# Kernel optimization log

Hardware: AMD Instinct MI355X
Metric: run time of the kernel (lower is better)

## Reference

```python
import jax, jax.numpy as jnp
import numpy as np

LATDIM = 128
HEAD = 4
N_NODES = 100000
N_EDGES = 800000

def setup_inputs() -> dict:
    key = jax.random.key(0)
    k1, k2, k3, k4, k5, k6 = jax.random.split(key, 6)
    scale = float(np.sqrt(6.0 / (LATDIM + LATDIM)))  # xavier_uniform bound
    return {
        "rows": jax.random.randint(k1, (N_EDGES,), 0, N_NODES),
        "colEmbeds": jax.random.normal(k2, (N_EDGES, LATDIM), dtype=jnp.float32),
        "embeds": jax.random.normal(k3, (N_NODES, LATDIM), dtype=jnp.float32),
        "qTrans": jax.random.uniform(k4, (LATDIM, LATDIM), minval=-scale, maxval=scale, dtype=jnp.float32),
        "kTrans": jax.random.uniform(k5, (LATDIM, LATDIM), minval=-scale, maxval=scale, dtype=jnp.float32),
        "vTrans": jax.random.uniform(k6, (LATDIM, LATDIM), minval=-scale, maxval=scale, dtype=jnp.float32),
        "shape": N_NODES,
    }

def reference(rows, colEmbeds, embeds, qTrans, kTrans, vTrans, shape):
    d_head = LATDIM // HEAD
    rowEmbeds = embeds[rows]                                   # [E, D] gather
    q = (rowEmbeds @ qTrans).reshape(-1, HEAD, d_head)          # [E, H, d]
    k = (colEmbeds @ kTrans).reshape(-1, HEAD, d_head)          # [E, H, d]
    v = (colEmbeds @ vTrans).reshape(-1, HEAD, d_head)          # [E, H, d]
    att = jnp.einsum('ehd,ehd->eh', q, k)                       # [E, H]
    att = jnp.clip(att, -10.0, 10.0)
    expAtt = jnp.exp(att)
    # segment softmax denominator, broadcast back to edges
    attNorm = jax.ops.segment_sum(expAtt, rows, num_segments=shape)[rows]
    att = expAtt / (attNorm + 1e-8)
    res = (att[:, :, None] * v).reshape(-1, LATDIM)             # [E, D]
    out = jax.ops.segment_sum(res, rows, num_segments=shape)    # [N, D]
    return out
```

## Files before the change

### kernel.cpp

```cpp
#include <hip/hip_runtime.h>
#include <hip/hip_bf16.h>

#define NEDGE 800000
#define NNODE 100000
#define LATD  128
#define NHEAD 4
#define WPAD  136
#define TILES (NEDGE / 16)
#define QTILES (NNODE / 16)
#define NB ((NNODE + 1023) / 1024)

typedef _Float16 half8 __attribute__((ext_vector_type(8)));
typedef _Float16 half4t __attribute__((ext_vector_type(4)));
typedef float    f32x4 __attribute__((ext_vector_type(4)));

__device__ __forceinline__ half8 load_frag_f32(const float* __restrict__ p) {
    const f32x4 a = *reinterpret_cast<const f32x4*>(p);
    const f32x4 b = *reinterpret_cast<const f32x4*>(p + 4);
    half8 r;
    r[0] = (_Float16)a[0]; r[1] = (_Float16)a[1];
    r[2] = (_Float16)a[2]; r[3] = (_Float16)a[3];
    r[4] = (_Float16)b[0]; r[5] = (_Float16)b[1];
    r[6] = (_Float16)b[2]; r[7] = (_Float16)b[3];
    return r;
}

__global__ __launch_bounds__(512, 2) void q_kernel(
    const float* __restrict__ embeds,
    const float* __restrict__ Qw,
    _Float16* __restrict__ qAll)
{
    extern __shared__ _Float16 lds[];
    _Float16* Qt = lds;
    const int t = threadIdx.x;
    for (int idx = t; idx < LATD * LATD; idx += 512) {
        const int d = idx >> 7, c = idx & 127;
        Qt[c * WPAD + d] = (_Float16)Qw[idx];
    }
    __syncthreads();

    const int lane = t & 63;
    const int c16  = lane & 15;
    const int g    = lane >> 4;
    const int wave = (blockIdx.x << 3) + (t >> 6);
    const int nw   = gridDim.x << 3;

    for (int tile = wave; tile < QTILES; tile += nw) {
        const int n0 = tile << 4;
        const float* xrow = embeds + (size_t)(n0 + c16) * LATD + g * 8;
        f32x4 accQ[8] = {};
        #pragma unroll
        for (int ks = 0; ks < 4; ++ks) {
            const half8 ax = load_frag_f32(xrow + ks * 32);
            const int ko = ks * 32 + g * 8;
            #pragma unroll
            for (int nt = 0; nt < 8; ++nt) {
                const half8 bq = *reinterpret_cast<const half8*>(Qt + (nt * 16 + c16) * WPAD + ko);
                accQ[nt] = __builtin_amdgcn_mfma_f32_16x16x32_f16(ax, bq, accQ[nt], 0, 0, 0);
            }
        }
        #pragma unroll
        for (int r = 0; r < 4; ++r) {
            half8 h;
            #pragma unroll
            for (int nt = 0; nt < 8; ++nt) h[nt] = (_Float16)accQ[nt][r];
            *reinterpret_cast<half8*>(qAll + (size_t)(n0 + g * 4 + r) * LATD + c16 * 8) = h;
        }
    }
}

__global__ void hist_kernel(const int* __restrict__ rows, int* __restrict__ counts) {
    const int e = blockIdx.x * 256 + threadIdx.x;
    if (e < NEDGE) atomicAdd(&counts[rows[e]], 1);
}

__global__ __launch_bounds__(1024) void scan1_kernel(
    const int* __restrict__ counts, int* __restrict__ offsets, int* __restrict__ partials)
{
    __shared__ int wt[16];
    __shared__ int wp[16];
    const int b = blockIdx.x;
    const int i = b * 1024 + threadIdx.x;
    const int v = (i < NNODE) ? counts[i] : 0;
    const int lane = threadIdx.x & 63, wid = threadIdx.x >> 6;
    int incl = v;
    #pragma unroll
    for (int d = 1; d < 64; d <<= 1) {
        const int x = __shfl_up(incl, d);
        if (lane >= d) incl += x;
    }
    if (lane == 63) wt[wid] = incl;
    __syncthreads();
    if (threadIdx.x == 0) {
        int s = 0;
        for (int k = 0; k < 16; ++k) { wp[k] = s; s += wt[k]; }
        partials[b] = s;
    }
    __syncthreads();
    if (i < NNODE) offsets[i] = incl - v + wp[wid];
}

__global__ __launch_bounds__(1024) void scan2_kernel(
    int* __restrict__ offsets, int* __restrict__ cursor, const int* __restrict__ partials)
{
    __shared__ int sp[128];
    const int b = blockIdx.x;
    if (threadIdx.x < NB) sp[threadIdx.x] = partials[threadIdx.x];
    __syncthreads();
    int s = 0;
    for (int k = 0; k < b; ++k) s += sp[k];
    const int i = b * 1024 + threadIdx.x;
    if (i < NNODE) {
        const int val = offsets[i] + s;
        offsets[i] = val;
        cursor[i]  = val;
    }
    if (b == 0 && threadIdx.x == 0) offsets[NNODE] = NEDGE;
}

__global__ void scatter_kernel(const int* __restrict__ rows,
                               int* __restrict__ cursor,
                               int* __restrict__ edgeIdx,
                               int* __restrict__ rowsSorted) {
    const int e = blockIdx.x * 256 + threadIdx.x;
    if (e < NEDGE) {
        const int r = rows[e];
        const int p = atomicAdd(&cursor[r], 1);
        edgeIdx[p]    = e;
        rowsSorted[p] = r;
    }
}

__global__ __launch_bounds__(512, 2) void att_kernel(
    const int*      __restrict__ rows,
    const float*    __restrict__ colEmb,
    const _Float16* __restrict__ qAll,
    const float*    __restrict__ Kw,
    _Float16* __restrict__ attN)
{
    extern __shared__ _Float16 lds[];
    _Float16* Kt = lds;
    const int t = threadIdx.x;
    for (int idx = t; idx < LATD * LATD; idx += 512) {
        const int d = idx >> 7, c = idx & 127;
        Kt[c * WPAD + d] = (_Float16)Kw[idx];
    }
    __syncthreads();

    const int lane = t & 63;
    const int c16  = lane & 15;
    const int g    = lane >> 4;
    const int wave = blockIdx.x * 8 + (t >> 6);
    const int nw   = gridDim.x * 8;

    for (int tile = wave; tile < TILES; tile += nw) {
        const int e0 = tile << 4;
        const float* yrow = colEmb + (size_t)(e0 + c16) * LATD + g * 8;

        half8 ay[4];
        #pragma unroll
        for (int ks = 0; ks < 4; ++ks) ay[ks] = load_frag_f32(yrow + ks * 32);

        const int4 rW = *reinterpret_cast<const int4*>(rows + e0 + g * 4);
        half8 qv[4];
        qv[0] = *reinterpret_cast<const half8*>(qAll + (size_t)rW.x * LATD + c16 * 8);
        qv[1] = *reinterpret_cast<const half8*>(qAll + (size_t)rW.y * LATD + c16 * 8);
        qv[2] = *reinterpret_cast<const half8*>(qAll + (size_t)rW.z * LATD + c16 * 8);
        qv[3] = *reinterpret_cast<const half8*>(qAll + (size_t)rW.w * LATD + c16 * 8);

        f32x4 accK[8] = {};
        #pragma unroll
        for (int ks = 0; ks < 4; ++ks) {
            const int ko = ks * 32 + g * 8;
            #pragma unroll
            for (int nt = 0; nt < 8; ++nt) {
                const half8 bk = *reinterpret_cast<const half8*>(Kt + (nt * 16 + c16) * WPAD + ko);
                accK[nt] = __builtin_amdgcn_mfma_f32_16x16x32_f16(ay[ks], bk, accK[nt], 0, 0, 0);
            }
        }

        f32x4 eh[4];
        #pragma unroll
        for (int h = 0; h < 4; ++h) {
            f32x4 p;
            #pragma unroll
            for (int r = 0; r < 4; ++r)
                p[r] = accK[2 * h][r]     * (float)qv[r][2 * h]
                     + accK[2 * h + 1][r] * (float)qv[r][2 * h + 1];
            #pragma unroll
            for (int m = 1; m < 16; m <<= 1) {
                f32x4 q;
                q[0] = __shfl_xor(p[0], m);
                q[1] = __shfl_xor(p[1], m);
                q[2] = __shfl_xor(p[2], m);
                q[3] = __shfl_xor(p[3], m);
                p += q;
            }
            #pragma unroll
            for (int r = 0; r < 4; ++r)
                eh[h][r] = expf(fminf(10.0f, fmaxf(-10.0f, p[r])));
        }

        const f32x4 sel = (c16 == 0) ? eh[0] : (c16 == 1) ? eh[1] : (c16 == 2) ? eh[2] : eh[3];
        if (c16 < NHEAD) {
            #pragma unroll
            for (int r = 0; r < 4; ++r)
                attN[(size_t)(e0 + 4 * g + r) * NHEAD + c16] = (_Float16)sel[r];
        }
    }
}

__global__ __launch_bounds__(512, 2) void pv_kernel(
    const int*      __restrict__ edgeIdx,
    const int*      __restrict__ rowsSorted,
    const float*    __restrict__ colEmb,
    const _Float16* __restrict__ attN,
    const float*    __restrict__ Vw,
    float* __restrict__ outAcc,
    float* __restrict__ attNorm,
    int tilesPerWave)
{
    extern __shared__ _Float16 lds[];
    _Float16* Vt = lds;
    const int t = threadIdx.x;
    for (int idx = t; idx < LATD * LATD; idx += 512) {
        const int d = idx >> 7, c = idx & 127;
        Vt[c * WPAD + d] = (_Float16)Vw[idx];
    }
    __syncthreads();

    const int lane = t & 63;
    const int c16  = lane & 15;
    const int g    = lane >> 4;
    const int wave = blockIdx.x * 8 + (t >> 6);
    const int tile0 = wave * tilesPerWave;
    int tile1 = tile0 + tilesPerWave;
    if (tile1 > TILES) tile1 = TILES;
    if (tile0 >= tile1) return;

    int eA      = edgeIdx[(tile0 << 4) + c16];
    int rid16   = rowsSorted[(tile0 << 4) + c16];
    int4 rB     = *reinterpret_cast<const int4*>(rowsSorted + (tile0 << 4) + g * 4);
    int4 eB     = *reinterpret_cast<const int4*>(edgeIdx    + (tile0 << 4) + g * 4);
    int prevRow = (g == 0) ? -1 : rowsSorted[(tile0 << 4) + 4 * g - 1];

    for (int tile = tile0; tile < tile1; ++tile) {
        const float* yrow = colEmb + (size_t)eA * LATD + g * 8;
        half8 ay[4];
        #pragma unroll
        for (int ks = 0; ks < 4; ++ks) ay[ks] = load_frag_f32(yrow + ks * 32);

        half4t a4[4];
        a4[0] = *reinterpret_cast<const half4t*>(attN + (size_t)eB.x * NHEAD);
        a4[1] = *reinterpret_cast<const half4t*>(attN + (size_t)eB.y * NHEAD);
        a4[2] = *reinterpret_cast<const half4t*>(attN + (size_t)eB.z * NHEAD);
        a4[3] = *reinterpret_cast<const half4t*>(attN + (size_t)eB.w * NHEAD);

        const bool hasNext = (tile + 1 < tile1);
        int eAn = 0, rid16n = 0, prevRowN = 0;
        int4 rBn = rB, eBn = eB;
        if (hasNext) {
            const int i1 = (tile + 1) << 4;
            eAn     = edgeIdx[i1 + c16];
            rid16n  = rowsSorted[i1 + c16];
            rBn     = *reinterpret_cast<const int4*>(rowsSorted + i1 + g * 4);
            eBn     = *reinterpret_cast<const int4*>(edgeIdx    + i1 + g * 4);
            prevRowN = (g == 0) ? -1 : rowsSorted[i1 + 4 * g - 1];
        }

        f32x4 accV[8] = {};
        #pragma unroll
        for (int ks = 0; ks < 4; ++ks) {
            const int ko = ks * 32 + g * 8;
            #pragma unroll
            for (int nt = 0; nt < 8; ++nt) {
                const half8 bv = *reinterpret_cast<const half8*>(Vt + (nt * 16 + c16) * WPAD + ko);
                accV[nt] = __builtin_amdgcn_mfma_f32_16x16x32_f16(ay[ks], bv, accV[nt], 0, 0, 0);
            }
        }

        half8 Pf = {};
        Pf[0] = (rB.x == rid16) ? (_Float16)1.f : (_Float16)0.f;
        Pf[1] = (rB.y == rid16) ? (_Float16)1.f : (_Float16)0.f;
        Pf[2] = (rB.z == rid16) ? (_Float16)1.f : (_Float16)0.f;
        Pf[3] = (rB.w == rid16) ? (_Float16)1.f : (_Float16)0.f;

        const f32x4 zero4 = {};
        #pragma unroll
        for (int nt = 0; nt < 8; ++nt) {
            const int h = nt >> 1;
            half8 Wf = {};
            Wf[0] = (_Float16)(accV[nt][0] * (float)a4[0][h] * 0.015625f);
            Wf[1] = (_Float16)(accV[nt][1] * (float)a4[1][h] * 0.015625f);
            Wf[2] = (_Float16)(accV[nt][2] * (float)a4[2][h] * 0.015625f);
            Wf[3] = (_Float16)(accV[nt][3] * (float)a4[3][h] * 0.015625f);
            accV[nt] = __builtin_amdgcn_mfma_f32_16x16x32_f16(Pf, Wf, zero4, 0, 0, 0);
        }
        half8 Df = {};
        if (c16 < NHEAD) {
            Df[0] = a4[0][c16]; Df[1] = a4[1][c16];
            Df[2] = a4[2][c16]; Df[3] = a4[3][c16];
        }
        const f32x4 Dden = __builtin_amdgcn_mfma_f32_16x16x32_f16(Pf, Df, zero4, 0, 0, 0);

        #pragma unroll
        for (int r = 0; r < 4; ++r) {
            const int cur = (r == 0) ? rB.x : (r == 1) ? rB.y : (r == 2) ? rB.z : rB.w;
            const int prv = (r == 0) ? prevRow : (r == 1) ? rB.x : (r == 2) ? rB.y : rB.z;
            if (cur != prv) {
                #pragma unroll
                for (int nt = 0; nt < 8; ++nt)
                    atomicAdd(outAcc + (size_t)cur * LATD + nt * 16 + c16, accV[nt][r] * 64.0f);
                if (c16 < NHEAD) atomicAdd(attNorm + cur * NHEAD + c16, Dden[r]);
            }
        }

        if (hasNext) { eA = eAn; rid16 = rid16n; rB = rBn; eB = eBn; prevRow = prevRowN; }
    }
}

__global__ void norm_kernel(float* __restrict__ out, const float* __restrict__ attNorm) {
    const int i = blockIdx.x * 256 + threadIdx.x;
    if (i >= NNODE * 32) return;
    const int n = i >> 5;
    const int h = (i & 31) >> 3;
    const float s = attNorm[n * NHEAD + h] + 1e-8f;
    f32x4* p = reinterpret_cast<f32x4*>(out) + i;
    f32x4 v = *p;
    v[0] /= s; v[1] /= s; v[2] /= s; v[3] /= s;
    *p = v;
}

__global__ __launch_bounds__(512, 2) void edge_kernel(
    const int*   __restrict__ rows,
    const float* __restrict__ colEmb,
    const float* __restrict__ embeds,
    const float* __restrict__ Qw,
    const float* __restrict__ Kw,
    const float* __restrict__ Vw,
    float* __restrict__ outAcc,
    float* __restrict__ attNorm)
{
    extern __shared__ _Float16 lds[];
    _Float16* Qt = lds;
    _Float16* Kt = lds + LATD * WPAD;
    _Float16* Vt = lds + 2 * LATD * WPAD;
    const int t = threadIdx.x;
    for (int idx = t; idx < LATD * LATD; idx += 512) {
        const int d = idx >> 7, c = idx & 127;
        Qt[c * WPAD + d] = (_Float16)Qw[idx];
        Kt[c * WPAD + d] = (_Float16)Kw[idx];
        Vt[c * WPAD + d] = (_Float16)Vw[idx];
    }
    __syncthreads();
    const int lane = t & 63;
    const int c16  = lane & 15;
    const int g    = lane >> 4;
    const int wave = (blockIdx.x << 3) + (t >> 6);
    const int nw   = gridDim.x << 3;
    for (int tile = wave; tile < TILES; tile += nw) {
        const int e0 = tile << 4;
        const int eA = e0 + c16;
        const int rA = rows[eA];
        const float* xrow = embeds + (size_t)rA * LATD + g * 8;
        const float* yrow = colEmb + (size_t)eA * LATD + g * 8;
        half8 ay[4];
        f32x4 accQ[8] = {};
        f32x4 accK[8] = {};
        #pragma unroll
        for (int ks = 0; ks < 4; ++ks) {
            const int ko = ks * 32 + g * 8;
            const half8 ax = load_frag_f32(xrow + ks * 32);
            ay[ks] = load_frag_f32(yrow + ks * 32);
            #pragma unroll
            for (int nt = 0; nt < 8; ++nt) {
                const int rofs = (nt * 16 + c16) * WPAD + ko;
                const half8 bq = *reinterpret_cast<const half8*>(Qt + rofs);
                const half8 bk = *reinterpret_cast<const half8*>(Kt + rofs);
                accQ[nt] = __builtin_amdgcn_mfma_f32_16x16x32_f16(ax,     bq, accQ[nt], 0, 0, 0);
                accK[nt] = __builtin_amdgcn_mfma_f32_16x16x32_f16(ay[ks], bk, accK[nt], 0, 0, 0);
            }
        }
        f32x4 eh[4];
        #pragma unroll
        for (int h = 0; h < 4; ++h) {
            f32x4 p = accQ[2 * h] * accK[2 * h] + accQ[2 * h + 1] * accK[2 * h + 1];
            #pragma unroll
            for (int m = 1; m < 16; m <<= 1) {
                f32x4 q;
                q[0] = __shfl_xor(p[0], m);
                q[1] = __shfl_xor(p[1], m);
                q[2] = __shfl_xor(p[2], m);
                q[3] = __shfl_xor(p[3], m);
                p += q;
            }
            #pragma unroll
            for (int r = 0; r < 4; ++r)
                eh[h][r] = expf(fminf(10.0f, fmaxf(-10.0f, p[r])));
        }
        int rB[4];
        #pragma unroll
        for (int r = 0; r < 4; ++r) rB[r] = rows[e0 + g * 4 + r];
        if (c16 < NHEAD) {
            const f32x4 sel = (c16 == 0) ? eh[0] : (c16 == 1) ? eh[1] : (c16 == 2) ? eh[2] : eh[3];
            #pragma unroll
            for (int r = 0; r < 4; ++r)
                atomicAdd(attNorm + rB[r] * NHEAD + c16, sel[r]);
        }
        f32x4 accV[8] = {};
        #pragma unroll
        for (int ks = 0; ks < 4; ++ks) {
            const int ko = ks * 32 + g * 8;
            #pragma unroll
            for (int nt = 0; nt < 8; ++nt) {
                const half8 bv = *reinterpret_cast<const half8*>(Vt + (nt * 16 + c16) * WPAD + ko);
                accV[nt] = __builtin_amdgcn_mfma_f32_16x16x32_f16(ay[ks], bv, accV[nt], 0, 0, 0);
            }
        }
        #pragma unroll
        for (int nt = 0; nt < 8; ++nt) {
            const f32x4 w = accV[nt] * eh[nt >> 1];
            #pragma unroll
            for (int r = 0; r < 4; ++r)
                atomicAdd(outAcc + (size_t)rB[r] * LATD + nt * 16 + c16, w[r]);
        }
    }
}

extern "C" void kernel_launch(void* const* d_in, const int* in_sizes, int n_in,
                              void* d_out, int out_size, void* d_ws, size_t ws_size,
                              hipStream_t stream) {
    const int*   rows   = (const int*)d_in[0];
    const float* colEmb = (const float*)d_in[1];
    const float* embeds = (const float*)d_in[2];
    const float* Qw     = (const float*)d_in[3];
    const float* Kw     = (const float*)d_in[4];
    const float* Vw     = (const float*)d_in[5];
    float* out = (float*)d_out;

    const size_t qAllB = (size_t)NNODE * LATD * sizeof(_Float16);
    const size_t cntB  = 400128;
    const size_t offB  = 402176;
    const size_t curB  = 400128;
    const size_t eidxB = (size_t)NEDGE * sizeof(int);
    const size_t rsrtB = (size_t)NEDGE * sizeof(int);
    const size_t partB = 512;
    const size_t attNB = (size_t)NEDGE * NHEAD * sizeof(_Float16);
    const size_t attB  = (size_t)NNODE * NHEAD * sizeof(float);
    const size_t needB = qAllB + cntB + offB + curB + eidxB + rsrtB + partB + attNB + attB;

    if (ws_size >= needB) {
        char* w = (char*)d_ws;
        _Float16* qAll    = (_Float16*)w; w += qAllB;
        int*   counts     = (int*)w;    w += cntB;
        int*   offsets    = (int*)w;    w += offB;
        int*   cursor     = (int*)w;    w += curB;
        int*   edgeIdx    = (int*)w;    w += eidxB;
        int*   rowsSorted = (int*)w;    w += rsrtB;
        int*   partials   = (int*)w;    w += partB;
        _Float16* attN    = (_Float16*)w; w += attNB;
        float* attNorm    = (float*)w;

        hipMemsetAsync(counts,  0, (size_t)NNODE * sizeof(int), stream);
        hipMemsetAsync(out,     0, (size_t)NNODE * LATD * sizeof(float), stream);
        hipMemsetAsync(attNorm, 0, (size_t)NNODE * NHEAD * sizeof(float), stream);

        const int ldsQ = LATD * WPAD * sizeof(_Float16);
        hipFuncSetAttribute((const void*)q_kernel,
                            hipFuncAttributeMaxDynamicSharedMemorySize, ldsQ);
        q_kernel<<<(QTILES + 7) / 8, 512, ldsQ, stream>>>(embeds, Qw, qAll);

        hist_kernel<<<(NEDGE + 255) / 256, 256, 0, stream>>>(rows, counts);
        scan1_kernel<<<NB, 1024, 0, stream>>>(counts, offsets, partials);
        scan2_kernel<<<NB, 1024, 0, stream>>>(offsets, cursor, partials);
        scatter_kernel<<<(NEDGE + 255) / 256, 256, 0, stream>>>(rows, cursor, edgeIdx, rowsSorted);

        hipFuncSetAttribute((const void*)att_kernel,
                            hipFuncAttributeMaxDynamicSharedMemorySize, ldsQ);
        att_kernel<<<1024, 512, ldsQ, stream>>>(rows, colEmb, qAll, Kw, attN);

        hipFuncSetAttribute((const void*)pv_kernel,
                            hipFuncAttributeMaxDynamicSharedMemorySize, ldsQ);
        const int nWaves = 1024 * 8;
        const int tpw = (TILES + nWaves - 1) / nWaves;
        pv_kernel<<<1024, 512, ldsQ, stream>>>(
            edgeIdx, rowsSorted, colEmb, attN, Vw, out, attNorm, tpw);

        const int nVec = NNODE * 32;
        norm_kernel<<<(nVec + 255) / 256, 256, 0, stream>>>(out, attNorm);
    } else {
        float* attNorm = (float*)d_ws;
        const int ldsBytes = 3 * LATD * WPAD * sizeof(_Float16);
        hipMemsetAsync(out,     0, (size_t)NNODE * LATD  * sizeof(float), stream);
        hipMemsetAsync(attNorm, 0, (size_t)NNODE * NHEAD * sizeof(float), stream);
        hipFuncSetAttribute((const void*)edge_kernel,
                            hipFuncAttributeMaxDynamicSharedMemorySize, ldsBytes);
        edge_kernel<<<512, 512, ldsBytes, stream>>>(rows, colEmb, embeds, Qw, Kw, Vw, out, attNorm);
        const int nVec = NNODE * 32;
        norm_kernel<<<(nVec + 255) / 256, 256, 0, stream>>>(out, attNorm);
    }
}
```

Before: 414.2 us.

## Write attention weights in sorted order and use plain stores for complete segments

The scatter kernel now records each edge's sorted position (rank), and the attention kernel writes exp-scores straight into sorted order. The PV kernel can then read attention weights contiguously instead of gathering them through edgeIdx. The PV kernel also uses ballots to find segment heads, and for row segments that start and end inside one tile it writes output and denominators with plain stores instead of atomics. The cost is an extra rank array, scattered writes in the attention kernel, and more complex boundary logic that relies on out and attNorm being zeroed.

```diff
diff --git a/kernel.cpp b/kernel.cpp
--- a/kernel.cpp
+++ b/kernel.cpp
@@ -121,18 +121,21 @@
 __global__ void scatter_kernel(const int* __restrict__ rows,
                                int* __restrict__ cursor,
                                int* __restrict__ edgeIdx,
-                               int* __restrict__ rowsSorted) {
+                               int* __restrict__ rowsSorted,
+                               int* __restrict__ rank) {
     const int e = blockIdx.x * 256 + threadIdx.x;
     if (e < NEDGE) {
         const int r = rows[e];
         const int p = atomicAdd(&cursor[r], 1);
         edgeIdx[p]    = e;
         rowsSorted[p] = r;
+        rank[e]       = p;
     }
 }
 
 __global__ __launch_bounds__(512, 2) void att_kernel(
     const int*      __restrict__ rows,
+    const int*      __restrict__ rank,
     const float*    __restrict__ colEmb,
     const _Float16* __restrict__ qAll,
     const float*    __restrict__ Kw,
@@ -203,9 +206,11 @@
 
         const f32x4 sel = (c16 == 0) ? eh[0] : (c16 == 1) ? eh[1] : (c16 == 2) ? eh[2] : eh[3];
         if (c16 < NHEAD) {
-            #pragma unroll
-            for (int r = 0; r < 4; ++r)
-                attN[(size_t)(e0 + 4 * g + r) * NHEAD + c16] = (_Float16)sel[r];
+            const int4 rk = *reinterpret_cast<const int4*>(rank + e0 + g * 4);
+            attN[(size_t)rk.x * NHEAD + c16] = (_Float16)sel[0];
+            attN[(size_t)rk.y * NHEAD + c16] = (_Float16)sel[1];
+            attN[(size_t)rk.z * NHEAD + c16] = (_Float16)sel[2];
+            attN[(size_t)rk.w * NHEAD + c16] = (_Float16)sel[3];
         }
     }
 }
@@ -238,34 +243,35 @@
     if (tile1 > TILES) tile1 = TILES;
     if (tile0 >= tile1) return;
 
-    int eA      = edgeIdx[(tile0 << 4) + c16];
-    int rid16   = rowsSorted[(tile0 << 4) + c16];
-    int4 rB     = *reinterpret_cast<const int4*>(rowsSorted + (tile0 << 4) + g * 4);
-    int4 eB     = *reinterpret_cast<const int4*>(edgeIdx    + (tile0 << 4) + g * 4);
-    int prevRow = (g == 0) ? -1 : rowsSorted[(tile0 << 4) + 4 * g - 1];
+    int eA    = edgeIdx[(tile0 << 4) + c16];
+    int rid16 = rowsSorted[(tile0 << 4) + c16];
+    int4 rB   = *reinterpret_cast<const int4*>(rowsSorted + (tile0 << 4) + g * 4);
 
     for (int tile = tile0; tile < tile1; ++tile) {
+        const int e0 = tile << 4;
+
         const float* yrow = colEmb + (size_t)eA * LATD + g * 8;
         half8 ay[4];
         #pragma unroll
         for (int ks = 0; ks < 4; ++ks) ay[ks] = load_frag_f32(yrow + ks * 32);
 
         half4t a4[4];
-        a4[0] = *reinterpret_cast<const half4t*>(attN + (size_t)eB.x * NHEAD);
-        a4[1] = *reinterpret_cast<const half4t*>(attN + (size_t)eB.y * NHEAD);
-        a4[2] = *reinterpret_cast<const half4t*>(attN + (size_t)eB.z * NHEAD);
-        a4[3] = *reinterpret_cast<const half4t*>(attN + (size_t)eB.w * NHEAD);
+        a4[0] = *reinterpret_cast<const half4t*>(attN + (size_t)(e0 + 4 * g + 0) * NHEAD);
+        a4[1] = *reinterpret_cast<const half4t*>(attN + (size_t)(e0 + 4 * g + 1) * NHEAD);
+        a4[2] = *reinterpret_cast<const half4t*>(attN + (size_t)(e0 + 4 * g + 2) * NHEAD);
+        a4[3] = *reinterpret_cast<const half4t*>(attN + (size_t)(e0 + 4 * g + 3) * NHEAD);
+
+        const int pPrev  = (e0 + 4 * g == 0) ? -1 : rowsSorted[e0 + 4 * g - 1];
+        const int nextRow = (e0 + 16 < NEDGE) ? rowsSorted[e0 + 16] : -1;
 
         const bool hasNext = (tile + 1 < tile1);
-        int eAn = 0, rid16n = 0, prevRowN = 0;
-        int4 rBn = rB, eBn = eB;
+        int eAn = 0, rid16n = 0;
+        int4 rBn = rB;
         if (hasNext) {
             const int i1 = (tile + 1) << 4;
-            eAn     = edgeIdx[i1 + c16];
-            rid16n  = rowsSorted[i1 + c16];
-            rBn     = *reinterpret_cast<const int4*>(rowsSorted + i1 + g * 4);
-            eBn     = *reinterpret_cast<const int4*>(edgeIdx    + i1 + g * 4);
-            prevRowN = (g == 0) ? -1 : rowsSorted[i1 + 4 * g - 1];
+            eAn    = edgeIdx[i1 + c16];
+            rid16n = rowsSorted[i1 + c16];
+            rBn    = *reinterpret_cast<const int4*>(rowsSorted + i1 + g * 4);
         }
 
         f32x4 accV[8] = {};
@@ -277,6 +283,23 @@
                 const half8 bv = *reinterpret_cast<const half8*>(Vt + (nt * 16 + c16) * WPAD + ko);
                 accV[nt] = __builtin_amdgcn_mfma_f32_16x16x32_f16(ay[ks], bv, accV[nt], 0, 0, 0);
             }
+        }
+
+        const bool h0 = (rB.x != pPrev);
+        const bool h1 = (rB.y != rB.x);
+        const bool h2 = (rB.z != rB.y);
+        const bool h3 = (rB.w != rB.z);
+        const unsigned long long m0 = __ballot(h0);
+        const unsigned long long m1 = __ballot(h1);
+        const unsigned long long m2 = __ballot(h2);
+        const unsigned long long m3 = __ballot(h3);
+        unsigned hm = 0;
+        #pragma unroll
+        for (int gg = 0; gg < 4; ++gg) {
+            hm |= (unsigned)((m0 >> (gg * 16)) & 1ULL) << (4 * gg + 0);
+            hm |= (unsigned)((m1 >> (gg * 16)) & 1ULL) << (4 * gg + 1);
+            hm |= (unsigned)((m2 >> (gg * 16)) & 1ULL) << (4 * gg + 2);
+            hm |= (unsigned)((m3 >> (gg * 16)) & 1ULL) << (4 * gg + 3);
         }
 
         half8 Pf = {};
@@ -305,17 +328,26 @@
 
         #pragma unroll
         for (int r = 0; r < 4; ++r) {
+            const int i = 4 * g + r;
             const int cur = (r == 0) ? rB.x : (r == 1) ? rB.y : (r == 2) ? rB.z : rB.w;
-            const int prv = (r == 0) ? prevRow : (r == 1) ? rB.x : (r == 2) ? rB.y : rB.z;
-            if (cur != prv) {
-                #pragma unroll
-                for (int nt = 0; nt < 8; ++nt)
-                    atomicAdd(outAcc + (size_t)cur * LATD + nt * 16 + c16, accV[nt][r] * 64.0f);
-                if (c16 < NHEAD) atomicAdd(attNorm + cur * NHEAD + c16, Dden[r]);
-            }
-        }
-
-        if (hasNext) { eA = eAn; rid16 = rid16n; rB = rBn; eB = eBn; prevRow = prevRowN; }
+            const bool isHead = (hm >> i) & 1;
+            if (isHead || i == 0) {
+                const bool complete = isHead && (((hm >> (i + 1)) != 0) || (nextRow != cur));
+                if (complete) {
+                    #pragma unroll
+                    for (int nt = 0; nt < 8; ++nt)
+                        outAcc[(size_t)cur * LATD + nt * 16 + c16] = accV[nt][r] * 64.0f;
+                    if (c16 < NHEAD) attNorm[cur * NHEAD + c16] = Dden[r];
+                } else {
+                    #pragma unroll
+                    for (int nt = 0; nt < 8; ++nt)
+                        atomicAdd(outAcc + (size_t)cur * LATD + nt * 16 + c16, accV[nt][r] * 64.0f);
+                    if (c16 < NHEAD) atomicAdd(attNorm + cur * NHEAD + c16, Dden[r]);
+                }
+            }
+        }
+
+        if (hasNext) { eA = eAn; rid16 = rid16n; rB = rBn; }
     }
 }
 
@@ -444,10 +476,11 @@
     const size_t curB  = 400128;
     const size_t eidxB = (size_t)NEDGE * sizeof(int);
     const size_t rsrtB = (size_t)NEDGE * sizeof(int);
+    const size_t rnkB  = (size_t)NEDGE * sizeof(int);
     const size_t partB = 512;
     const size_t attNB = (size_t)NEDGE * NHEAD * sizeof(_Float16);
     const size_t attB  = (size_t)NNODE * NHEAD * sizeof(float);
-    const size_t needB = qAllB + cntB + offB + curB + eidxB + rsrtB + partB + attNB + attB;
+    const size_t needB = qAllB + cntB + offB + curB + eidxB + rsrtB + rnkB + partB + attNB + attB;
 
     if (ws_size >= needB) {
         char* w = (char*)d_ws;
@@ -457,6 +490,7 @@
         int*   cursor     = (int*)w;    w += curB;
         int*   edgeIdx    = (int*)w;    w += eidxB;
         int*   rowsSorted = (int*)w;    w += rsrtB;
+        int*   rank       = (int*)w;    w += rnkB;
         int*   partials   = (int*)w;    w += partB;
         _Float16* attN    = (_Float16*)w; w += attNB;
         float* attNorm    = (float*)w;
@@ -473,11 +507,11 @@
         hist_kernel<<<(NEDGE + 255) / 256, 256, 0, stream>>>(rows, counts);
         scan1_kernel<<<NB, 1024, 0, stream>>>(counts, offsets, partials);
         scan2_kernel<<<NB, 1024, 0, stream>>>(offsets, cursor, partials);
-        scatter_kernel<<<(NEDGE + 255) / 256, 256, 0, stream>>>(rows, cursor, edgeIdx, rowsSorted);
+        scatter_kernel<<<(NEDGE + 255) / 256, 256, 0, stream>>>(rows, cursor, edgeIdx, rowsSorted, rank);
 
         hipFuncSetAttribute((const void*)att_kernel,
                             hipFuncAttributeMaxDynamicSharedMemorySize, ldsQ);
-        att_kernel<<<1024, 512, ldsQ, stream>>>(rows, colEmb, qAll, Kw, attN);
+        att_kernel<<<1024, 512, ldsQ, stream>>>(rows, rank, colEmb, qAll, Kw, attN);
 
         hipFuncSetAttribute((const void*)pv_kernel,
                             hipFuncAttributeMaxDynamicSharedMemorySize, ldsQ);
```

Result: no change. 418.7 us (+1.1%).
